# Kernel tuning notes

Hardware: AMD Instinct MI355X
Metric: run time of the kernel (lower is better)

Reference implementation:

```python
import jax, jax.numpy as jnp
import numpy as np

NC = 80          # classes
REG_MAX = 16     # DFL bins
NK = 51          # 17*3 keypoint channels
KPT_SHAPE = (17, 3)
MAX_DET = 100
CONF_THRES = 0.25
STRIDES = (8, 16, 32)


def _conv1x1(f, w, b):
    # f: (B,C,H,W), w: (O,C), b: (O,) -> (B,O,H,W)
    return jnp.einsum('bchw,oc->bohw', f, w) + b[None, :, None, None]


def _make_anchors(shapes, strides, offset=0.5):
    pts, sts = [], []
    for (h, w), s in zip(shapes, strides):
        sx = jnp.arange(w, dtype=jnp.float32) + offset
        sy = jnp.arange(h, dtype=jnp.float32) + offset
        gy, gx = jnp.meshgrid(sy, sx, indexing='ij')
        pts.append(jnp.stack([gx, gy], -1).reshape(-1, 2))
        sts.append(jnp.full((h * w, 1), float(s), jnp.float32))
    # transposed as in _new_inference: anchors (2,A), strides (1,A)
    return jnp.concatenate(pts, 0).T, jnp.concatenate(sts, 0).T


def setup_inputs() -> dict:
    key = jax.random.key(0)
    ks = jax.random.split(key, 16)
    ch = (128, 256, 512)
    hw = ((80, 80), (40, 40), (20, 20))
    d = {}
    for i, (c, (h, w)) in enumerate(zip(ch, hw)):
        d[f'x{i}'] = jax.random.normal(ks[i], (16, c, h, w), jnp.float32)
    k = 3
    for name, oc in (('cv2', 4 * REG_MAX), ('cv3', NC), ('cv4', NK)):
        for i, c in enumerate(ch):
            d[f'{name}_w{i}'] = jax.random.normal(ks[k], (oc, c), jnp.float32) * 0.02
            d[f'{name}_b{i}'] = jnp.zeros((oc,), jnp.float32)
            k += 1
    return d


def reference(x0, x1, x2,
              cv2_w0, cv2_b0, cv2_w1, cv2_b1, cv2_w2, cv2_b2,
              cv3_w0, cv3_b0, cv3_w1, cv3_b1, cv3_w2, cv3_b2,
              cv4_w0, cv4_b0, cv4_w1, cv4_b1, cv4_w2, cv4_b2):
    feats = [x0, x1, x2]
    cv2 = [(cv2_w0, cv2_b0), (cv2_w1, cv2_b1), (cv2_w2, cv2_b2)]
    cv3 = [(cv3_w0, cv3_b0), (cv3_w1, cv3_b1), (cv3_w2, cv3_b2)]
    cv4 = [(cv4_w0, cv4_b0), (cv4_w1, cv4_b1), (cv4_w2, cv4_b2)]
    bs = x0.shape[0]

    # keypoint branch: cat over levels -> (bs, nk, A)
    kpt = jnp.concatenate(
        [_conv1x1(f, w, b).reshape(bs, NK, -1) for f, (w, b) in zip(feats, cv4)], -1)
    # box+cls branch -> (bs, 4*reg_max+nc, A)
    xcat = jnp.concatenate(
        [jnp.concatenate([_conv1x1(f, *cv2[i]), _conv1x1(f, *cv3[i])], 1).reshape(bs, 4 * REG_MAX + NC, -1)
         for i, f in enumerate(feats)], -1)
    box, cls = xcat[:, :4 * REG_MAX], xcat[:, 4 * REG_MAX:]

    shapes = [(f.shape[2], f.shape[3]) for f in feats]
    anchors, strides = _make_anchors(shapes, STRIDES)  # (2,A), (1,A)
    A = anchors.shape[1]

    # DFL decode: softmax over reg_max bins, expectation w/ arange weights
    p = jax.nn.softmax(box.reshape(bs, 4, REG_MAX, A), axis=2)
    dist = jnp.einsum('bfra,r->bfa', p, jnp.arange(REG_MAX, dtype=jnp.float32))
    lt, rb = dist[:, :2], dist[:, 2:]
    x1y1 = anchors[None] - lt
    x2y2 = anchors[None] + rb
    # xywh box coding, scaled by strides
    dbox = jnp.concatenate([(x1y1 + x2y2) * 0.5, x2y2 - x1y1], 1) * strides[None]  # (bs,4,A)

    # keypoint decode (Pose.kpts_decode, ndim==3)
    y = kpt.reshape(bs, KPT_SHAPE[0], KPT_SHAPE[1], A)
    kxy = (y[:, :, :2] * 2.0 + (anchors[None, None] - 0.5)) * strides[None, None]
    kv = jax.nn.sigmoid(y[:, :, 2:3])
    pred_kpts = jnp.concatenate([kxy, kv], 2).reshape(bs, NK, A).transpose(0, 2, 1)  # (bs,A,nk)

    # EfficientIdxNMS_TRT stand-in: sigmoid scores (score_activation=1),
    # class-agnostic deterministic top-k selection by best class score.
    scores = jax.nn.sigmoid(cls.transpose(0, 2, 1))  # (bs,A,nc)
    max_s = scores.max(-1)
    cls_id = jnp.argmax(scores, -1)
    top_s, top_i = jax.lax.top_k(max_s, MAX_DET)     # (bs,MAX_DET)
    num_dets = (top_s > CONF_THRES).sum(-1).astype(jnp.int32)[:, None]
    det_boxes = jnp.take_along_axis(dbox.transpose(0, 2, 1), top_i[..., None], 1)  # (bs,MAX_DET,4)
    det_classes = jnp.take_along_axis(cls_id, top_i, 1).astype(jnp.int32)
    # irregular keypoint gather via det indices (the pred_kpts[bs_indices, det_indices] step)
    det_kpts = jnp.take_along_axis(pred_kpts, top_i[..., None], 1).reshape(bs, MAX_DET, *KPT_SHAPE)
    return num_dets, det_boxes, top_s, det_classes, det_kpts
```

## Files before the change

kernel.cpp:

```cpp
#include <hip/hip_runtime.h>
#include <hip/hip_bf16.h>

#define NC 80
#define NK 51
#define REG_MAX 16
#define MAX_DET 100
#define A_TOT 8400
#define BS 16

#define OUT_NUM 0
#define OUT_BOX 16
#define OUT_SCORE (16 + 16*MAX_DET*4)
#define OUT_CLASS (OUT_SCORE + 16*MAX_DET)
#define OUT_KPT (OUT_CLASS + 16*MAX_DET)

static __device__ __forceinline__ unsigned long long mk_key(unsigned u, int a) {
    return ((unsigned long long)u << 32) | (unsigned)(0x7FFFFFFF - a);
}

__global__ __launch_bounds__(256) void scores_fused(
    const float* __restrict__ x0, const float* __restrict__ x1, const float* __restrict__ x2,
    const float* __restrict__ w0, const float* __restrict__ w1, const float* __restrict__ w2,
    const float* __restrict__ bias0, const float* __restrict__ bias1, const float* __restrict__ bias2,
    float* __restrict__ max_s,
    int* __restrict__ cls_id)
{
    __shared__ float fs[32 * 128];
    __shared__ float wsh[80 * 32];
    __shared__ float rm[4][128];
    __shared__ int   ri[4][128];

    int bid = blockIdx.x;
    const float *x, *w, *bias; int C, A, a_off, b, tile;
    if (bid < 64) {
        x = x2; w = w2; bias = bias2; C = 512; A = 400; a_off = 8000;
        b = bid >> 2; tile = bid & 3;
    } else if (bid < 272) {
        int r = bid - 64;
        x = x1; w = w1; bias = bias1; C = 256; A = 1600; a_off = 6400;
        b = r / 13; tile = r - b * 13;
    } else {
        int r = bid - 272;
        x = x0; w = w0; bias = bias0; C = 128; A = 6400; a_off = 0;
        b = r / 50; tile = r - b * 50;
    }
    int a0 = tile * 128;

    int t = threadIdx.x;
    int lane = t & 63;
    int wv = t >> 6;
    int oc0 = wv * 20;

    float acc0[20], acc1[20];
#pragma unroll
    for (int j = 0; j < 20; ++j) { float bv = bias[oc0 + j]; acc0[j] = bv; acc1[j] = bv; }

    const float* xb = x + (long)b * C * A;
    int nchunk = C >> 5;

    for (int kc = 0; kc < nchunk; ++kc) {
        __syncthreads();
#pragma unroll
        for (int i = 0; i < 4; ++i) {
            int idx = t + i * 256;
            int c = idx >> 5;
            int q = (idx & 31) * 4;
            int aa = a0 + q; if (aa > A - 4) aa = A - 4;
            float4 v = *(const float4*)(xb + (long)(kc * 32 + c) * A + aa);
            *(float4*)(&fs[c * 128 + q]) = v;
        }
#pragma unroll
        for (int i = 0; i < 3; ++i) {
            int idx = t + i * 256;
            if (idx < 640) {
                int oc = idx >> 3;
                int q = (idx & 7) * 4;
                float4 v = *(const float4*)(w + oc * C + kc * 32 + q);
                *(float4*)(&wsh[oc * 32 + q]) = v;
            }
        }
        __syncthreads();

#pragma unroll 1
        for (int c4 = 0; c4 < 32; c4 += 4) {
            float fa[4], fb[4];
#pragma unroll
            for (int cc = 0; cc < 4; ++cc) {
                fa[cc] = fs[(c4 + cc) * 128 + lane];
                fb[cc] = fs[(c4 + cc) * 128 + lane + 64];
            }
#pragma unroll
            for (int j = 0; j < 20; ++j) {
                float4 w4 = *(const float4*)(&wsh[(oc0 + j) * 32 + c4]);
                acc0[j] = fmaf(w4.x, fa[0], acc0[j]);
                acc0[j] = fmaf(w4.y, fa[1], acc0[j]);
                acc0[j] = fmaf(w4.z, fa[2], acc0[j]);
                acc0[j] = fmaf(w4.w, fa[3], acc0[j]);
                acc1[j] = fmaf(w4.x, fb[0], acc1[j]);
                acc1[j] = fmaf(w4.y, fb[1], acc1[j]);
                acc1[j] = fmaf(w4.z, fb[2], acc1[j]);
                acc1[j] = fmaf(w4.w, fb[3], acc1[j]);
            }
        }
    }

    float m0 = acc0[0], m1 = acc1[0]; int i0 = 0, i1 = 0;
#pragma unroll
    for (int j = 1; j < 20; ++j) {
        if (acc0[j] > m0) { m0 = acc0[j]; i0 = j; }
        if (acc1[j] > m1) { m1 = acc1[j]; i1 = j; }
    }
    i0 += oc0; i1 += oc0;

    rm[wv][lane] = m0;      ri[wv][lane] = i0;
    rm[wv][lane + 64] = m1; ri[wv][lane + 64] = i1;
    __syncthreads();
    if (wv == 0) {
#pragma unroll
        for (int p = 0; p < 2; ++p) {
            int a = lane + p * 64;
            float bm = rm[0][a]; int bi = ri[0][a];
#pragma unroll
            for (int v = 1; v < 4; ++v) {
                float om = rm[v][a];
                if (om > bm) { bm = om; bi = ri[v][a]; }
            }
            int ga = a0 + a;
            if (ga < A) {
                max_s[b * A_TOT + a_off + ga] = 1.0f / (1.0f + expf(-bm));
                cls_id[b * A_TOT + a_off + ga] = bi;
            }
        }
    }
}

__global__ __launch_bounds__(1024) void topk_kernel(
    const float* __restrict__ max_s,
    const int* __restrict__ cls_id,
    float* __restrict__ out,
    int* __restrict__ top_idx)
{
    int b = blockIdx.x;
    int t = threadIdx.x;
    int wv = t >> 6;

    __shared__ unsigned hist[16 * 256];
    __shared__ unsigned suffix[256];
    __shared__ int tieIdx[A_TOT];
    __shared__ unsigned long long highKeys[128];
    __shared__ unsigned long long finalKeys[128];
    __shared__ int wmin[16];
    __shared__ unsigned s_prefix;
    __shared__ int s_k, s_selD, s_nHigh, s_nTie, s_cnt, s_bcast;

    unsigned u[9];
    bool val[9];
#pragma unroll
    for (int i = 0; i < 9; ++i) {
        int a = t + i * 1024;
        val[i] = (a < A_TOT);
        u[i] = val[i] ? __float_as_uint(max_s[b * A_TOT + a]) : 0u;
    }

    if (t == 0) { s_prefix = 0; s_k = MAX_DET; s_nHigh = 0; s_nTie = 0; s_cnt = 0; }

    for (int pass = 0; pass < 4; ++pass) {
#pragma unroll
        for (int j = 0; j < 4; ++j) hist[t + j * 1024] = 0;
        if (t == 0) s_selD = 0;
        __syncthreads();

        unsigned pre = s_prefix;
        int k = s_k;
        int shHi = 32 - 8 * pass;
        int shD = 24 - 8 * pass;
#pragma unroll
        for (int i = 0; i < 9; ++i) {
            if (val[i]) {
                bool cand = (pass == 0) ? true : ((u[i] >> shHi) == pre);
                if (cand)
                    atomicAdd(&hist[(wv << 8) + ((u[i] >> shD) & 0xFF)], 1u);
            }
        }
        __syncthreads();

        if (t < 256) {
            unsigned s = 0;
#pragma unroll
            for (int w = 0; w < 16; ++w) s += hist[(w << 8) + t];
            suffix[t] = s;
        }
        __syncthreads();
        for (int off = 1; off < 256; off <<= 1) {
            unsigned v = 0;
            if (t < 256) v = suffix[t] + ((t + off < 256) ? suffix[t + off] : 0u);
            __syncthreads();
            if (t < 256) suffix[t] = v;
            __syncthreads();
        }
        if (t < 256 && suffix[t] >= (unsigned)k) atomicMax(&s_selD, t);
        __syncthreads();
        if (t == 0) {
            int d = s_selD;
            s_k = k - ((d < 255) ? (int)suffix[d + 1] : 0);
            s_prefix = (pre << 8) | (unsigned)d;
        }
        __syncthreads();
    }

    unsigned cut = s_prefix;
    int r = s_k;

#pragma unroll
    for (int i = 0; i < 9; ++i) {
        if (val[i]) {
            int a = t + i * 1024;
            if (u[i] > cut) {
                int p = atomicAdd(&s_nHigh, 1);
                highKeys[p] = mk_key(u[i], a);
            } else if (u[i] == cut) {
                int p = atomicAdd(&s_nTie, 1);
                tieIdx[p] = a;
            }
        }
    }
    __syncthreads();
    int m = s_nHigh;
    int nt = s_nTie;

    if (t < 128) finalKeys[t] = 0ull;
    __syncthreads();
    if (t < m) finalKeys[t] = highKeys[t];

    if (nt == r) {
        if (t < nt) finalKeys[m + t] = mk_key(cut, tieIdx[t]);
        __syncthreads();
    } else {
        __syncthreads();
        for (int j = 0; j < r; ++j) {
            int mn = 0x7FFFFFFF;
            for (int p = t; p < nt; p += 1024) mn = min(mn, tieIdx[p]);
            for (int off = 32; off > 0; off >>= 1) mn = min(mn, __shfl_down(mn, off, 64));
            if ((t & 63) == 0) wmin[wv] = mn;
            __syncthreads();
            if (t == 0) {
                int v = wmin[0];
#pragma unroll
                for (int w = 1; w < 16; ++w) v = min(v, wmin[w]);
                s_bcast = v;
                finalKeys[m + j] = mk_key(cut, v);
            }
            __syncthreads();
            int v = s_bcast;
            for (int p = t; p < nt; p += 1024)
                if (tieIdx[p] == v) tieIdx[p] = 0x7FFFFFFF;
            __syncthreads();
        }
    }

    for (int ksz = 2; ksz <= 128; ksz <<= 1) {
        for (int j = ksz >> 1; j > 0; j >>= 1) {
            if (t < 128) {
                int ixj = t ^ j;
                if (ixj > t) {
                    bool desc = ((t & ksz) == 0);
                    unsigned long long x = finalKeys[t], y = finalKeys[ixj];
                    bool sw = desc ? (x < y) : (x > y);
                    if (sw) { finalKeys[t] = y; finalKeys[ixj] = x; }
                }
            }
            __syncthreads();
        }
    }

    if (t < MAX_DET) {
        unsigned long long kk = finalKeys[t];
        float sc = __uint_as_float((unsigned)(kk >> 32));
        int a = 0x7FFFFFFF - (int)(kk & 0xFFFFFFFFull);
        out[OUT_SCORE + b * MAX_DET + t] = sc;
        out[OUT_CLASS + b * MAX_DET + t] = (float)cls_id[b * A_TOT + a];
        top_idx[b * MAX_DET + t] = a;
        if (sc > 0.25f) atomicAdd(&s_cnt, 1);
    }
    __syncthreads();
    if (t == 0) out[OUT_NUM + b] = (float)s_cnt;
}

__global__ __launch_bounds__(128) void decode_kernel(
    const float* __restrict__ x0, const float* __restrict__ x1, const float* __restrict__ x2,
    const float* __restrict__ w2_0, const float* __restrict__ b2_0,
    const float* __restrict__ w2_1, const float* __restrict__ b2_1,
    const float* __restrict__ w2_2, const float* __restrict__ b2_2,
    const float* __restrict__ w4_0, const float* __restrict__ b4_0,
    const float* __restrict__ w4_1, const float* __restrict__ b4_1,
    const float* __restrict__ w4_2, const float* __restrict__ b4_2,
    const int* __restrict__ top_idx,
    float* __restrict__ out)
{
    int b = blockIdx.y;
    int k = blockIdx.x;
    int a = top_idx[b * MAX_DET + k];

    const float* x; const float* w2; const float* bb2; const float* w4; const float* bb4;
    int C, A, W, a_local; float stride;
    if (a < 6400)      { x = x0; C = 128; A = 6400; W = 80; stride = 8.0f;  a_local = a;        w2 = w2_0; bb2 = b2_0; w4 = w4_0; bb4 = b4_0; }
    else if (a < 8000) { x = x1; C = 256; A = 1600; W = 40; stride = 16.0f; a_local = a - 6400; w2 = w2_1; bb2 = b2_1; w4 = w4_1; bb4 = b4_1; }
    else               { x = x2; C = 512; A = 400;  W = 20; stride = 32.0f; a_local = a - 8000; w2 = w2_2; bb2 = b2_2; w4 = w4_2; bb4 = b4_2; }

    __shared__ float fs[512];
    __shared__ float logits[64];
    __shared__ float kraw[NK];
    __shared__ float dist[4];

    int t = threadIdx.x;
    for (int c = t; c < C; c += 128)
        fs[c] = x[((long)b * C + c) * A + a_local];
    __syncthreads();

    if (t < 64 + NK) {
        const float* wrow; float acc;
        if (t < 64) { wrow = w2 + t * C; acc = bb2[t]; }
        else        { wrow = w4 + (t - 64) * C; acc = bb4[t - 64]; }
        for (int c = 0; c < C; ++c) acc = fmaf(wrow[c], fs[c], acc);
        if (t < 64) logits[t] = acc;
        else        kraw[t - 64] = acc;
    }
    __syncthreads();

    if (t < 4) {
        float mx = logits[t * 16];
#pragma unroll
        for (int r = 1; r < 16; ++r) mx = fmaxf(mx, logits[t * 16 + r]);
        float se = 0.0f, sw = 0.0f;
#pragma unroll
        for (int r = 0; r < 16; ++r) {
            float e = expf(logits[t * 16 + r] - mx);
            se += e; sw += e * (float)r;
        }
        dist[t] = sw / se;
    }
    __syncthreads();

    float ax = (float)(a_local % W) + 0.5f;
    float ay = (float)(a_local / W) + 0.5f;

    if (t == 0) {
        float x1c = ax - dist[0], y1c = ay - dist[1];
        float x2c = ax + dist[2], y2c = ay + dist[3];
        float* ob = out + OUT_BOX + ((long)b * MAX_DET + k) * 4;
        ob[0] = (x1c + x2c) * 0.5f * stride;
        ob[1] = (y1c + y2c) * 0.5f * stride;
        ob[2] = (x2c - x1c) * stride;
        ob[3] = (y2c - y1c) * stride;
    }
    if (t < 17) {
        float vx = kraw[t * 3], vy = kraw[t * 3 + 1], vv = kraw[t * 3 + 2];
        float gx = ax - 0.5f, gy = ay - 0.5f;
        float* ok = out + OUT_KPT + (((long)b * MAX_DET + k) * 17 + t) * 3;
        ok[0] = (vx * 2.0f + gx) * stride;
        ok[1] = (vy * 2.0f + gy) * stride;
        ok[2] = 1.0f / (1.0f + expf(-vv));
    }
}

extern "C" void kernel_launch(void* const* d_in, const int* in_sizes, int n_in,
                              void* d_out, int out_size, void* d_ws, size_t ws_size,
                              hipStream_t stream) {
    const float* x0 = (const float*)d_in[0];
    const float* x1 = (const float*)d_in[1];
    const float* x2 = (const float*)d_in[2];
    const float* w2[3] = {(const float*)d_in[3], (const float*)d_in[5], (const float*)d_in[7]};
    const float* b2[3] = {(const float*)d_in[4], (const float*)d_in[6], (const float*)d_in[8]};
    const float* w3[3] = {(const float*)d_in[9], (const float*)d_in[11], (const float*)d_in[13]};
    const float* b3[3] = {(const float*)d_in[10], (const float*)d_in[12], (const float*)d_in[14]};
    const float* w4[3] = {(const float*)d_in[15], (const float*)d_in[17], (const float*)d_in[19]};
    const float* b4[3] = {(const float*)d_in[16], (const float*)d_in[18], (const float*)d_in[20]};

    float* out = (float*)d_out;

    float* ws_maxs = (float*)d_ws;
    int* ws_cls = (int*)(ws_maxs + BS * A_TOT);
    int* ws_top = (int*)(ws_cls + BS * A_TOT);

    scores_fused<<<dim3(1072), 256, 0, stream>>>(
        x0, x1, x2, w3[0], w3[1], w3[2], b3[0], b3[1], b3[2], ws_maxs, ws_cls);
    topk_kernel<<<dim3(BS), 1024, 0, stream>>>(ws_maxs, ws_cls, out, ws_top);
    decode_kernel<<<dim3(MAX_DET, BS), 128, 0, stream>>>(
        x0, x1, x2,
        w2[0], b2[0], w2[1], b2[1], w2[2], b2[2],
        w4[0], b4[0], w4[1], b4[1], w4[2], b4[2],
        ws_top, out);
}
```

Measured before the change: 307.4 us.

## Restructure class-score GEMM to register-resident weights broadcast via readlane

```diff
diff --git a/kernel.cpp b/kernel.cpp
--- a/kernel.cpp
+++ b/kernel.cpp
@@ -18,118 +18,126 @@
     return ((unsigned long long)u << 32) | (unsigned)(0x7FFFFFFF - a);
 }
 
-__global__ __launch_bounds__(256) void scores_fused(
+__global__ __launch_bounds__(512) void scores_fused(
     const float* __restrict__ x0, const float* __restrict__ x1, const float* __restrict__ x2,
     const float* __restrict__ w0, const float* __restrict__ w1, const float* __restrict__ w2,
     const float* __restrict__ bias0, const float* __restrict__ bias1, const float* __restrict__ bias2,
     float* __restrict__ max_s,
     int* __restrict__ cls_id)
 {
-    __shared__ float fs[32 * 128];
-    __shared__ float wsh[80 * 32];
-    __shared__ float rm[4][128];
-    __shared__ int   ri[4][128];
+    __shared__ float rm[8][256];
+    __shared__ int   ri[8][256];
 
     int bid = blockIdx.x;
     const float *x, *w, *bias; int C, A, a_off, b, tile;
-    if (bid < 64) {
+    if (bid < 32) {
         x = x2; w = w2; bias = bias2; C = 512; A = 400; a_off = 8000;
-        b = bid >> 2; tile = bid & 3;
-    } else if (bid < 272) {
-        int r = bid - 64;
+        b = bid >> 1; tile = bid & 1;
+    } else if (bid < 144) {
+        int r = bid - 32;
         x = x1; w = w1; bias = bias1; C = 256; A = 1600; a_off = 6400;
-        b = r / 13; tile = r - b * 13;
+        b = r / 7; tile = r - b * 7;
     } else {
-        int r = bid - 272;
+        int r = bid - 144;
         x = x0; w = w0; bias = bias0; C = 128; A = 6400; a_off = 0;
-        b = r / 50; tile = r - b * 50;
-    }
-    int a0 = tile * 128;
+        b = r / 25; tile = r - b * 25;
+    }
+    int a0 = tile * 256;
 
     int t = threadIdx.x;
     int lane = t & 63;
     int wv = t >> 6;
-    int oc0 = wv * 20;
-
-    float acc0[20], acc1[20];
-#pragma unroll
-    for (int j = 0; j < 20; ++j) { float bv = bias[oc0 + j]; acc0[j] = bv; acc1[j] = bv; }
-
-    const float* xb = x + (long)b * C * A;
+    int oc0 = wv * 10;
+
+    int aa = a0 + lane * 4; if (aa > A - 4) aa = A - 4;
+    const float* xb = x + (long)b * C * A + aa;
+
+    int wrow = oc0 + (lane >> 5);
+    int wcol = lane & 31;
+
+    float acc[10][4];
+#pragma unroll
+    for (int j = 0; j < 10; ++j) {
+        float bv = bias[oc0 + j];
+        acc[j][0] = bv; acc[j][1] = bv; acc[j][2] = bv; acc[j][3] = bv;
+    }
+
     int nchunk = C >> 5;
+    float wcur[5], wnxt[5];
+#pragma unroll
+    for (int r2 = 0; r2 < 5; ++r2)
+        wcur[r2] = w[(wrow + 2 * r2) * C + wcol];
 
     for (int kc = 0; kc < nchunk; ++kc) {
-        __syncthreads();
-#pragma unroll
-        for (int i = 0; i < 4; ++i) {
-            int idx = t + i * 256;
-            int c = idx >> 5;
-            int q = (idx & 31) * 4;
-            int aa = a0 + q; if (aa > A - 4) aa = A - 4;
-            float4 v = *(const float4*)(xb + (long)(kc * 32 + c) * A + aa);
-            *(float4*)(&fs[c * 128 + q]) = v;
-        }
-#pragma unroll
-        for (int i = 0; i < 3; ++i) {
-            int idx = t + i * 256;
-            if (idx < 640) {
-                int oc = idx >> 3;
-                int q = (idx & 7) * 4;
-                float4 v = *(const float4*)(w + oc * C + kc * 32 + q);
-                *(float4*)(&wsh[oc * 32 + q]) = v;
+        int cbase = kc * 32;
+        if (kc + 1 < nchunk) {
+#pragma unroll
+            for (int r2 = 0; r2 < 5; ++r2)
+                wnxt[r2] = w[(wrow + 2 * r2) * C + cbase + 32 + wcol];
+        }
+
+#pragma unroll 2
+        for (int c4 = 0; c4 < 32; c4 += 4) {
+            const float* fp = xb + (long)(cbase + c4) * A;
+            float4 f0 = *(const float4*)(fp);
+            float4 f1 = *(const float4*)(fp + A);
+            float4 f2 = *(const float4*)(fp + 2 * A);
+            float4 f3 = *(const float4*)(fp + 3 * A);
+#pragma unroll
+            for (int j = 0; j < 10; ++j) {
+                int rr = j >> 1;
+                int hi = (j & 1) << 5;
+                float ws0 = __int_as_float(__builtin_amdgcn_readlane(__float_as_int(wcur[rr]), hi + c4 + 0));
+                float ws1 = __int_as_float(__builtin_amdgcn_readlane(__float_as_int(wcur[rr]), hi + c4 + 1));
+                float ws2 = __int_as_float(__builtin_amdgcn_readlane(__float_as_int(wcur[rr]), hi + c4 + 2));
+                float ws3 = __int_as_float(__builtin_amdgcn_readlane(__float_as_int(wcur[rr]), hi + c4 + 3));
+                acc[j][0] = fmaf(ws0, f0.x, acc[j][0]);
+                acc[j][0] = fmaf(ws1, f1.x, acc[j][0]);
+                acc[j][0] = fmaf(ws2, f2.x, acc[j][0]);
+                acc[j][0] = fmaf(ws3, f3.x, acc[j][0]);
+                acc[j][1] = fmaf(ws0, f0.y, acc[j][1]);
+                acc[j][1] = fmaf(ws1, f1.y, acc[j][1]);
+                acc[j][1] = fmaf(ws2, f2.y, acc[j][1]);
+                acc[j][1] = fmaf(ws3, f3.y, acc[j][1]);
+                acc[j][2] = fmaf(ws0, f0.z, acc[j][2]);
+                acc[j][2] = fmaf(ws1, f1.z, acc[j][2]);
+                acc[j][2] = fmaf(ws2, f2.z, acc[j][2]);
+                acc[j][2] = fmaf(ws3, f3.z, acc[j][2]);
+                acc[j][3] = fmaf(ws0, f0.w, acc[j][3]);
+                acc[j][3] = fmaf(ws1, f1.w, acc[j][3]);
+                acc[j][3] = fmaf(ws2, f2.w, acc[j][3]);
+                acc[j][3] = fmaf(ws3, f3.w, acc[j][3]);
             }
         }
-        __syncthreads();
-
-#pragma unroll 1
-        for (int c4 = 0; c4 < 32; c4 += 4) {
-            float fa[4], fb[4];
-#pragma unroll
-            for (int cc = 0; cc < 4; ++cc) {
-                fa[cc] = fs[(c4 + cc) * 128 + lane];
-                fb[cc] = fs[(c4 + cc) * 128 + lane + 64];
-            }
-#pragma unroll
-            for (int j = 0; j < 20; ++j) {
-                float4 w4 = *(const float4*)(&wsh[(oc0 + j) * 32 + c4]);
-                acc0[j] = fmaf(w4.x, fa[0], acc0[j]);
-                acc0[j] = fmaf(w4.y, fa[1], acc0[j]);
-                acc0[j] = fmaf(w4.z, fa[2], acc0[j]);
-                acc0[j] = fmaf(w4.w, fa[3], acc0[j]);
-                acc1[j] = fmaf(w4.x, fb[0], acc1[j]);
-                acc1[j] = fmaf(w4.y, fb[1], acc1[j]);
-                acc1[j] = fmaf(w4.z, fb[2], acc1[j]);
-                acc1[j] = fmaf(w4.w, fb[3], acc1[j]);
-            }
-        }
-    }
-
-    float m0 = acc0[0], m1 = acc1[0]; int i0 = 0, i1 = 0;
-#pragma unroll
-    for (int j = 1; j < 20; ++j) {
-        if (acc0[j] > m0) { m0 = acc0[j]; i0 = j; }
-        if (acc1[j] > m1) { m1 = acc1[j]; i1 = j; }
-    }
-    i0 += oc0; i1 += oc0;
-
-    rm[wv][lane] = m0;      ri[wv][lane] = i0;
-    rm[wv][lane + 64] = m1; ri[wv][lane + 64] = i1;
-    __syncthreads();
-    if (wv == 0) {
-#pragma unroll
-        for (int p = 0; p < 2; ++p) {
-            int a = lane + p * 64;
-            float bm = rm[0][a]; int bi = ri[0][a];
-#pragma unroll
-            for (int v = 1; v < 4; ++v) {
-                float om = rm[v][a];
-                if (om > bm) { bm = om; bi = ri[v][a]; }
-            }
-            int ga = a0 + a;
-            if (ga < A) {
-                max_s[b * A_TOT + a_off + ga] = 1.0f / (1.0f + expf(-bm));
-                cls_id[b * A_TOT + a_off + ga] = bi;
-            }
+
+        if (kc + 1 < nchunk) {
+#pragma unroll
+            for (int r2 = 0; r2 < 5; ++r2) wcur[r2] = wnxt[r2];
+        }
+    }
+
+#pragma unroll
+    for (int q = 0; q < 4; ++q) {
+        float m = acc[0][q]; int mi = 0;
+#pragma unroll
+        for (int j = 1; j < 10; ++j)
+            if (acc[j][q] > m) { m = acc[j][q]; mi = j; }
+        rm[wv][lane * 4 + q] = m;
+        ri[wv][lane * 4 + q] = oc0 + mi;
+    }
+    __syncthreads();
+
+    if (t < 256) {
+        float bm = rm[0][t]; int bi = ri[0][t];
+#pragma unroll
+        for (int v = 1; v < 8; ++v) {
+            float om = rm[v][t];
+            if (om > bm) { bm = om; bi = ri[v][t]; }
+        }
+        int ga = a0 + t;
+        if (ga < A) {
+            max_s[b * A_TOT + a_off + ga] = 1.0f / (1.0f + expf(-bm));
+            cls_id[b * A_TOT + a_off + ga] = bi;
         }
     }
 }
@@ -382,7 +390,7 @@
     int* ws_cls = (int*)(ws_maxs + BS * A_TOT);
     int* ws_top = (int*)(ws_cls + BS * A_TOT);
 
-    scores_fused<<<dim3(1072), 256, 0, stream>>>(
+    scores_fused<<<dim3(544), 512, 0, stream>>>(
         x0, x1, x2, w3[0], w3[1], w3[2], b3[0], b3[1], b3[2], ws_maxs, ws_cls);
     topk_kernel<<<dim3(BS), 1024, 0, stream>>>(ws_maxs, ws_cls, out, ws_top);
     decode_kernel<<<dim3(MAX_DET, BS), 128, 0, stream>>>(
```

New measurement: 312.5 us. Within noise of the previous version (+1.7%).

## Shrink top-k block to 256 threads with wave-level histogram scan and vectorized loads

Applied to the files above, without the earlier changes.

```diff
diff --git a/kernel.cpp b/kernel.cpp
--- a/kernel.cpp
+++ b/kernel.cpp
@@ -134,7 +134,7 @@
     }
 }
 
-__global__ __launch_bounds__(1024) void topk_kernel(
+__global__ __launch_bounds__(256) void topk_kernel(
     const float* __restrict__ max_s,
     const int* __restrict__ cls_id,
     float* __restrict__ out,
@@ -142,32 +142,32 @@
 {
     int b = blockIdx.x;
     int t = threadIdx.x;
+    int lane = t & 63;
     int wv = t >> 6;
 
-    __shared__ unsigned hist[16 * 256];
-    __shared__ unsigned suffix[256];
+    __shared__ unsigned hist[4 * 256];
     __shared__ int tieIdx[A_TOT];
     __shared__ unsigned long long highKeys[128];
     __shared__ unsigned long long finalKeys[128];
-    __shared__ int wmin[16];
+    __shared__ int wmin[4];
     __shared__ unsigned s_prefix;
-    __shared__ int s_k, s_selD, s_nHigh, s_nTie, s_cnt, s_bcast;
-
-    unsigned u[9];
-    bool val[9];
+    __shared__ int s_k, s_nHigh, s_nTie, s_cnt, s_bcast;
+
+    uint4 uu[9];
 #pragma unroll
     for (int i = 0; i < 9; ++i) {
-        int a = t + i * 1024;
-        val[i] = (a < A_TOT);
-        u[i] = val[i] ? __float_as_uint(max_s[b * A_TOT + a]) : 0u;
+        int idx = t + i * 256;
+        if (i < 8 || t < 52)
+            uu[i] = *(const uint4*)((const unsigned*)(max_s + (long)b * A_TOT) + idx * 4);
+        else
+            uu[i] = make_uint4(0u, 0u, 0u, 0u);
     }
 
     if (t == 0) { s_prefix = 0; s_k = MAX_DET; s_nHigh = 0; s_nTie = 0; s_cnt = 0; }
 
     for (int pass = 0; pass < 4; ++pass) {
 #pragma unroll
-        for (int j = 0; j < 4; ++j) hist[t + j * 1024] = 0;
-        if (t == 0) s_selD = 0;
+        for (int j = 0; j < 4; ++j) hist[t + j * 256] = 0;
         __syncthreads();
 
         unsigned pre = s_prefix;
@@ -176,34 +176,55 @@
         int shD = 24 - 8 * pass;
 #pragma unroll
         for (int i = 0; i < 9; ++i) {
-            if (val[i]) {
-                bool cand = (pass == 0) ? true : ((u[i] >> shHi) == pre);
-                if (cand)
-                    atomicAdd(&hist[(wv << 8) + ((u[i] >> shD) & 0xFF)], 1u);
-            }
-        }
-        __syncthreads();
-
-        if (t < 256) {
-            unsigned s = 0;
-#pragma unroll
-            for (int w = 0; w < 16; ++w) s += hist[(w << 8) + t];
-            suffix[t] = s;
-        }
-        __syncthreads();
-        for (int off = 1; off < 256; off <<= 1) {
-            unsigned v = 0;
-            if (t < 256) v = suffix[t] + ((t + off < 256) ? suffix[t + off] : 0u);
-            __syncthreads();
-            if (t < 256) suffix[t] = v;
-            __syncthreads();
-        }
-        if (t < 256 && suffix[t] >= (unsigned)k) atomicMax(&s_selD, t);
-        __syncthreads();
-        if (t == 0) {
-            int d = s_selD;
-            s_k = k - ((d < 255) ? (int)suffix[d + 1] : 0);
-            s_prefix = (pre << 8) | (unsigned)d;
+            if (i < 8 || t < 52) {
+                unsigned e[4] = { uu[i].x, uu[i].y, uu[i].z, uu[i].w };
+#pragma unroll
+                for (int j = 0; j < 4; ++j) {
+                    bool cand = (pass == 0) ? true : ((e[j] >> shHi) == pre);
+                    if (cand)
+                        atomicAdd(&hist[(wv << 8) + ((e[j] >> shD) & 0xFF)], 1u);
+                }
+            }
+        }
+        __syncthreads();
+
+        if (wv == 0) {
+            unsigned c0 = 0, c1 = 0, c2 = 0, c3 = 0;
+#pragma unroll
+            for (int w = 0; w < 4; ++w) {
+                const unsigned* hp = &hist[(w << 8) + lane * 4];
+                c0 += hp[0]; c1 += hp[1]; c2 += hp[2]; c3 += hp[3];
+            }
+            unsigned s3 = c3, s2 = c2 + s3, s1 = c1 + s2, s0 = c0 + s1;
+            unsigned tsum = s0;
+#pragma unroll
+            for (int off = 1; off < 64; off <<= 1) {
+                unsigned o = __shfl_down(tsum, off, 64);
+                if (lane + off < 64) tsum += o;
+            }
+            unsigned excl = tsum - s0;
+            unsigned S0 = excl + s0, S1 = excl + s1, S2 = excl + s2, S3 = excl + s3;
+            int ld = -1;
+            unsigned uk = (unsigned)k;
+            if (S3 >= uk)      ld = lane * 4 + 3;
+            else if (S2 >= uk) ld = lane * 4 + 2;
+            else if (S1 >= uk) ld = lane * 4 + 1;
+            else if (S0 >= uk) ld = lane * 4 + 0;
+            int d = ld;
+#pragma unroll
+            for (int off = 32; off > 0; off >>= 1) d = max(d, __shfl_xor(d, off, 64));
+            int dn = d + 1;
+            unsigned mine = 0;
+            if (dn < 256 && lane == (dn >> 2)) {
+                int e = dn & 3;
+                mine = (e == 0) ? S0 : (e == 1) ? S1 : (e == 2) ? S2 : S3;
+            }
+#pragma unroll
+            for (int off = 32; off > 0; off >>= 1) mine += __shfl_xor(mine, off, 64);
+            if (lane == 0) {
+                s_k = k - (int)mine;
+                s_prefix = (pre << 8) | (unsigned)d;
+            }
         }
         __syncthreads();
     }
@@ -213,14 +234,18 @@
 
 #pragma unroll
     for (int i = 0; i < 9; ++i) {
-        if (val[i]) {
-            int a = t + i * 1024;
-            if (u[i] > cut) {
-                int p = atomicAdd(&s_nHigh, 1);
-                highKeys[p] = mk_key(u[i], a);
-            } else if (u[i] == cut) {
-                int p = atomicAdd(&s_nTie, 1);
-                tieIdx[p] = a;
+        if (i < 8 || t < 52) {
+            unsigned e[4] = { uu[i].x, uu[i].y, uu[i].z, uu[i].w };
+#pragma unroll
+            for (int j = 0; j < 4; ++j) {
+                int a = (t + i * 256) * 4 + j;
+                if (e[j] > cut) {
+                    int p = atomicAdd(&s_nHigh, 1);
+                    highKeys[p] = mk_key(e[j], a);
+                } else if (e[j] == cut) {
+                    int p = atomicAdd(&s_nTie, 1);
+                    tieIdx[p] = a;
+                }
             }
         }
     }
@@ -239,20 +264,18 @@
         __syncthreads();
         for (int j = 0; j < r; ++j) {
             int mn = 0x7FFFFFFF;
-            for (int p = t; p < nt; p += 1024) mn = min(mn, tieIdx[p]);
+            for (int p = t; p < nt; p += 256) mn = min(mn, tieIdx[p]);
             for (int off = 32; off > 0; off >>= 1) mn = min(mn, __shfl_down(mn, off, 64));
-            if ((t & 63) == 0) wmin[wv] = mn;
+            if (lane == 0) wmin[wv] = mn;
             __syncthreads();
             if (t == 0) {
-                int v = wmin[0];
-#pragma unroll
-                for (int w = 1; w < 16; ++w) v = min(v, wmin[w]);
+                int v = min(min(wmin[0], wmin[1]), min(wmin[2], wmin[3]));
                 s_bcast = v;
                 finalKeys[m + j] = mk_key(cut, v);
             }
             __syncthreads();
             int v = s_bcast;
-            for (int p = t; p < nt; p += 1024)
+            for (int p = t; p < nt; p += 256)
                 if (tieIdx[p] == v) tieIdx[p] = 0x7FFFFFFF;
             __syncthreads();
         }
@@ -321,7 +344,14 @@
         const float* wrow; float acc;
         if (t < 64) { wrow = w2 + t * C; acc = bb2[t]; }
         else        { wrow = w4 + (t - 64) * C; acc = bb4[t - 64]; }
-        for (int c = 0; c < C; ++c) acc = fmaf(wrow[c], fs[c], acc);
+        for (int c = 0; c < C; c += 4) {
+            float4 wv4 = *(const float4*)(wrow + c);
+            float4 fv4 = *(const float4*)(&fs[c]);
+            acc = fmaf(wv4.x, fv4.x, acc);
+            acc = fmaf(wv4.y, fv4.y, acc);
+            acc = fmaf(wv4.z, fv4.z, acc);
+            acc = fmaf(wv4.w, fv4.w, acc);
+        }
         if (t < 64) logits[t] = acc;
         else        kraw[t - 64] = acc;
     }
@@ -384,7 +414,7 @@
 
     scores_fused<<<dim3(1072), 256, 0, stream>>>(
         x0, x1, x2, w3[0], w3[1], w3[2], b3[0], b3[1], b3[2], ws_maxs, ws_cls);
-    topk_kernel<<<dim3(BS), 1024, 0, stream>>>(ws_maxs, ws_cls, out, ws_top);
+    topk_kernel<<<dim3(BS), 256, 0, stream>>>(ws_maxs, ws_cls, out, ws_top);
     decode_kernel<<<dim3(MAX_DET, BS), 128, 0, stream>>>(
         x0, x1, x2,
         w2[0], b2[0], w2[1], b2[1], w2[2], b2[2],
```

Result: faster. 300.4 us (-2.3%).
